# Optimization experiments

Hardware: AMD Instinct MI355X
Metric: run time of the kernel (lower is better)

## Reference

```python
import jax, jax.numpy as jnp
import numpy as np


def setup_inputs() -> dict:
    key = jax.random.key(0)
    k1, k2, k3, k4 = jax.random.split(key, 4)
    B, C, H, W = 16, 256, 64, 64
    OUT = 256
    x = jax.random.normal(k1, (B, C, H, W), dtype=jnp.float32)
    context = jax.random.normal(k2, (B, C, H, W), dtype=jnp.float32)
    # conv1: 1x1 Conv2d(in=C, out=OUT) -> weight [OUT, C], bias [OUT]
    w1 = jax.random.normal(k3, (OUT, C), dtype=jnp.float32) * (1.0 / np.sqrt(C))
    b1 = jax.random.normal(k4, (OUT,), dtype=jnp.float32) * 0.01
    return {"x": x, "context": context, "w1": w1, "b1": b1}


def reference(x, context, w1, b1):
    # AdaptiveAvgPool2d((1,1)) over context -> per-(b,c) scalar scale [B, C]
    scale = jnp.mean(context, axis=(2, 3))
    # grouped conv with groups=B*C and 1x1 kernels == per-channel elementwise scale
    depth_feat = x * scale[:, :, None, None]  # [B, C, H, W]
    # 1x1 pointwise conv: contract channel dim
    out = jnp.einsum("bchw,oc->bohw", depth_feat, w1) + b1[None, :, None, None]
    return out
```

## Files before the change

kernel.cpp:

```cpp
#include <hip/hip_runtime.h>
#include <hip/hip_bf16.h>


typedef __attribute__((ext_vector_type(8))) short short8;
typedef __attribute__((ext_vector_type(4))) float f32x4;
typedef __attribute__((ext_vector_type(4))) unsigned int u32x4;

static __device__ __forceinline__ unsigned int bfbits(float f) {
    unsigned int u = __float_as_uint(f);
    return u + 0x7FFFu + ((u >> 16) & 1u);
}

static __device__ __forceinline__ unsigned int pkbf(float lo, float hi) {
#if __has_builtin(__builtin_amdgcn_perm)
    return __builtin_amdgcn_perm(bfbits(hi), bfbits(lo), 0x07060302u);
#else
    return (bfbits(lo) >> 16) | (bfbits(hi) & 0xffff0000u);
#endif
}

__global__ __launch_bounds__(256) void scale_kernel(const float* __restrict__ ctx,
                                                    float* __restrict__ scale) {
    const int bc = blockIdx.x;
    const float4* p = (const float4*)(ctx + (size_t)bc * 4096);
    const int t = threadIdx.x;
    float s = 0.f;
#pragma unroll
    for (int k = 0; k < 4; k++) {
        float4 v = p[t + k * 256];
        s += v.x + v.y + v.z + v.w;
    }
#pragma unroll
    for (int off = 32; off > 0; off >>= 1) s += __shfl_down(s, off);
    __shared__ float ws[4];
    if ((t & 63) == 0) ws[t >> 6] = s;
    __syncthreads();
    if (t == 0) scale[bc] = (ws[0] + ws[1] + ws[2] + ws[3]) * (1.0f / 4096.0f);
}

__global__ __launch_bounds__(256) void w2f_kernel(const float* __restrict__ w1,
                                                  const float* __restrict__ scale,
                                                  unsigned short* __restrict__ w2f) {
    const int gt = blockIdx.x * 256 + threadIdx.x;
    const int lane = gt & 63;
    const int m16 = (gt >> 6) & 15;
    const int ks = (gt >> 10) & 7;
    const int b = gt >> 13;
    const int lr = lane & 15;
    const int g = lane >> 4;
    const int row = m16 * 16 + lr;
    const int c0 = ks * 32 + g * 8;

    const float* wr = w1 + row * 256 + c0;
    const float* sc = scale + b * 256 + c0;
    float4 wv0 = *(const float4*)(wr);
    float4 wv1 = *(const float4*)(wr + 4);
    float4 sv0 = *(const float4*)(sc);
    float4 sv1 = *(const float4*)(sc + 4);

    u32x4 pv;
    pv[0] = pkbf(wv0.x * sv0.x, wv0.y * sv0.y);
    pv[1] = pkbf(wv0.z * sv0.z, wv0.w * sv0.w);
    pv[2] = pkbf(wv1.x * sv1.x, wv1.y * sv1.y);
    pv[3] = pkbf(wv1.z * sv1.z, wv1.w * sv1.w);
    *(u32x4*)(w2f + (size_t)gt * 8) = pv;
}

__global__ __launch_bounds__(256, 4) void gemm_kernel(const float* __restrict__ x,
                                                      const unsigned short* __restrict__ w2f,
                                                      const float* __restrict__ b1,
                                                      float* __restrict__ out) {
    const int bid = blockIdx.x;
    const int b = bid >> 7;
    const int hw0 = (bid & 127) * 32;
    const int tid = threadIdx.x;
    const int w = tid >> 6;
    const int lane = tid & 63;
    const int g = lane >> 4;
    const int lr = lane & 15;
    const int o0 = (w & 1) * 128;
    const int cw = hw0 + (w >> 1) * 16;
    const int m16b = (w & 1) * 8;

    const unsigned short* Af = w2f + (size_t)b * 65536;
    const float* Xcol = x + (size_t)b * (256 * 4096) + cw + lr;

    f32x4 acc[8];
#pragma unroll
    for (int m = 0; m < 8; m++) acc[m] = (f32x4)(0.f);

    float bcur[8], bnxt[8];
#pragma unroll
    for (int e = 0; e < 8; e++) bcur[e] = Xcol[(size_t)(g * 8 + e) * 4096];

#pragma unroll
    for (int ks = 0; ks < 8; ks++) {
        if (ks < 7) {
#pragma unroll
            for (int e = 0; e < 8; e++)
                bnxt[e] = Xcol[(size_t)((ks + 1) * 32 + g * 8 + e) * 4096];
        }
        short8 a[8];
#pragma unroll
        for (int m = 0; m < 8; m++)
            a[m] = *(const short8*)(Af + ((size_t)(ks * 16 + m16b + m) * 64 + lane) * 8);
        u32x4 pv;
#pragma unroll
        for (int j = 0; j < 4; j++) pv[j] = pkbf(bcur[2 * j], bcur[2 * j + 1]);
        short8 bf = __builtin_bit_cast(short8, pv);
#pragma unroll
        for (int m = 0; m < 8; m++)
            acc[m] = __builtin_amdgcn_mfma_f32_16x16x32_bf16(a[m], bf, acc[m], 0, 0, 0);
#pragma unroll
        for (int e = 0; e < 8; e++) bcur[e] = bnxt[e];
    }

    float* outp = out + (size_t)b * 256 * 4096 + cw + lr;
#pragma unroll
    for (int m = 0; m < 8; m++) {
#pragma unroll
        for (int r = 0; r < 4; r++) {
            const int row = o0 + m * 16 + g * 4 + r;
            outp[(size_t)row * 4096] = acc[m][r] + b1[row];
        }
    }
}

extern "C" void kernel_launch(void* const* d_in, const int* in_sizes, int n_in,
                              void* d_out, int out_size, void* d_ws, size_t ws_size,
                              hipStream_t stream) {
    const float* x = (const float*)d_in[0];
    const float* context = (const float*)d_in[1];
    const float* w1 = (const float*)d_in[2];
    const float* b1 = (const float*)d_in[3];
    float* out = (float*)d_out;

    float* scale = (float*)d_ws;
    unsigned short* w2f = (unsigned short*)((char*)d_ws + 16384);

    scale_kernel<<<4096, 256, 0, stream>>>(context, scale);
    w2f_kernel<<<512, 256, 0, stream>>>(w1, scale, w2f);
    gemm_kernel<<<2048, 256, 0, stream>>>(x, w2f, b1, out);
}
```

Before: 51.52 us.

## Stage X tiles in LDS via async global_load_lds and switch to 32x32 MFMA

The GEMM now uses 64-column output tiles per block (half the grid). It loads X tiles into double-buffered shared memory with direct global-to-LDS loads, and uses 32x32x16 bf16 MFMAs with a 2x2 accumulator tile per wave. The weight pre-pack kernel is re-laid out to match the 32x32 fragment layout. This aims to coalesce X reads and raise MFMA efficiency, at the cost of 32KB LDS per block, block-level barriers and lower occupancy.

After: 42.49 us. -17.5%, faster.

```diff
diff --git a/kernel.cpp b/kernel.cpp
--- a/kernel.cpp
+++ b/kernel.cpp
@@ -3,7 +3,7 @@
 
 
 typedef __attribute__((ext_vector_type(8))) short short8;
-typedef __attribute__((ext_vector_type(4))) float f32x4;
+typedef __attribute__((ext_vector_type(16))) float f32x16;
 typedef __attribute__((ext_vector_type(4))) unsigned int u32x4;
 
 static __device__ __forceinline__ unsigned int bfbits(float f) {
@@ -17,6 +17,12 @@
 #else
     return (bfbits(lo) >> 16) | (bfbits(hi) & 0xffff0000u);
 #endif
+}
+
+static __device__ __forceinline__ void gload16(const void* g, void* l) {
+    __builtin_amdgcn_global_load_lds(
+        (const __attribute__((address_space(1))) unsigned int*)g,
+        (__attribute__((address_space(3))) unsigned int*)l, 16, 0, 0);
 }
 
 __global__ __launch_bounds__(256) void scale_kernel(const float* __restrict__ ctx,
@@ -42,14 +48,12 @@
                                                   const float* __restrict__ scale,
                                                   unsigned short* __restrict__ w2f) {
     const int gt = blockIdx.x * 256 + threadIdx.x;
-    const int lane = gt & 63;
-    const int m16 = (gt >> 6) & 15;
-    const int ks = (gt >> 10) & 7;
+    const int l = gt & 63;
+    const int mt = (gt >> 6) & 7;
+    const int ks = (gt >> 9) & 15;
     const int b = gt >> 13;
-    const int lr = lane & 15;
-    const int g = lane >> 4;
-    const int row = m16 * 16 + lr;
-    const int c0 = ks * 32 + g * 8;
+    const int row = mt * 32 + (l & 31);
+    const int c0 = ks * 16 + (l >> 5) * 8;
 
     const float* wr = w1 + row * 256 + c0;
     const float* sc = scale + b * 256 + c0;
@@ -66,64 +70,91 @@
     *(u32x4*)(w2f + (size_t)gt * 8) = pv;
 }
 
-__global__ __launch_bounds__(256, 4) void gemm_kernel(const float* __restrict__ x,
+__global__ __launch_bounds__(256, 3) void gemm_kernel(const float* __restrict__ x,
                                                       const unsigned short* __restrict__ w2f,
                                                       const float* __restrict__ b1,
                                                       float* __restrict__ out) {
+    __shared__ float bst[2][4096];
+
     const int bid = blockIdx.x;
-    const int b = bid >> 7;
-    const int hw0 = (bid & 127) * 32;
+    const int b = bid >> 6;
+    const int hw0 = (bid & 63) * 64;
     const int tid = threadIdx.x;
     const int w = tid >> 6;
     const int lane = tid & 63;
-    const int g = lane >> 4;
-    const int lr = lane & 15;
-    const int o0 = (w & 1) * 128;
-    const int cw = hw0 + (w >> 1) * 16;
-    const int m16b = (w & 1) * 8;
+    const int l31 = lane & 31;
+    const int lh = lane >> 5;
+    const int o0 = w * 64;
 
     const unsigned short* Af = w2f + (size_t)b * 65536;
-    const float* Xcol = x + (size_t)b * (256 * 4096) + cw + lr;
-
-    f32x4 acc[8];
-#pragma unroll
-    for (int m = 0; m < 8; m++) acc[m] = (f32x4)(0.f);
-
-    float bcur[8], bnxt[8];
-#pragma unroll
-    for (int e = 0; e < 8; e++) bcur[e] = Xcol[(size_t)(g * 8 + e) * 4096];
+    const float* Xb = x + (size_t)b * (256 * 4096) + hw0;
 
 #pragma unroll
-    for (int ks = 0; ks < 8; ks++) {
-        if (ks < 7) {
+    for (int i = 0; i < 4; i++) {
+        const int idx = i * 256 + tid;
+        gload16(Xb + (size_t)(idx >> 4) * 4096 + (idx & 15) * 4, &bst[0][idx * 4]);
+    }
+    __syncthreads();
+
+    f32x16 acc[2][2];
 #pragma unroll
-            for (int e = 0; e < 8; e++)
-                bnxt[e] = Xcol[(size_t)((ks + 1) * 32 + g * 8 + e) * 4096];
+    for (int mtl = 0; mtl < 2; mtl++)
+#pragma unroll
+        for (int ntl = 0; ntl < 2; ntl++) acc[mtl][ntl] = (f32x16)(0.f);
+
+    const int bbase = lh * 512 + l31;
+
+#pragma unroll
+    for (int kt = 0; kt < 4; kt++) {
+        if (kt < 3) {
+#pragma unroll
+            for (int i = 0; i < 4; i++) {
+                const int idx = i * 256 + tid;
+                gload16(Xb + (size_t)((kt + 1) * 64 + (idx >> 4)) * 4096 + (idx & 15) * 4,
+                        &bst[(kt + 1) & 1][idx * 4]);
+            }
         }
-        short8 a[8];
+        const float* bb = bst[kt & 1];
+
+        short8 a[4][2];
 #pragma unroll
-        for (int m = 0; m < 8; m++)
-            a[m] = *(const short8*)(Af + ((size_t)(ks * 16 + m16b + m) * 64 + lane) * 8);
-        u32x4 pv;
+        for (int sub = 0; sub < 4; sub++)
 #pragma unroll
-        for (int j = 0; j < 4; j++) pv[j] = pkbf(bcur[2 * j], bcur[2 * j + 1]);
-        short8 bf = __builtin_bit_cast(short8, pv);
+            for (int mtl = 0; mtl < 2; mtl++)
+                a[sub][mtl] = *(const short8*)(
+                    Af + (((size_t)(kt * 4 + sub) * 8 + (w * 2 + mtl)) * 64 + lane) * 8);
+
 #pragma unroll
-        for (int m = 0; m < 8; m++)
-            acc[m] = __builtin_amdgcn_mfma_f32_16x16x32_bf16(a[m], bf, acc[m], 0, 0, 0);
+        for (int sub = 0; sub < 4; sub++) {
 #pragma unroll
-        for (int e = 0; e < 8; e++) bcur[e] = bnxt[e];
+            for (int ntl = 0; ntl < 2; ntl++) {
+                float bf32[8];
+#pragma unroll
+                for (int e = 0; e < 8; e++)
+                    bf32[e] = bb[bbase + ntl * 32 + sub * 1024 + e * 64];
+                u32x4 pv;
+#pragma unroll
+                for (int j = 0; j < 4; j++) pv[j] = pkbf(bf32[2 * j], bf32[2 * j + 1]);
+                short8 bfr = __builtin_bit_cast(short8, pv);
+#pragma unroll
+                for (int mtl = 0; mtl < 2; mtl++)
+                    acc[mtl][ntl] = __builtin_amdgcn_mfma_f32_32x32x16_bf16(
+                        a[sub][mtl], bfr, acc[mtl][ntl], 0, 0, 0);
+            }
+        }
+        __syncthreads();
     }
 
-    float* outp = out + (size_t)b * 256 * 4096 + cw + lr;
+    float* outb = out + (size_t)b * 256 * 4096 + hw0;
 #pragma unroll
-    for (int m = 0; m < 8; m++) {
+    for (int mtl = 0; mtl < 2; mtl++)
 #pragma unroll
-        for (int r = 0; r < 4; r++) {
-            const int row = o0 + m * 16 + g * 4 + r;
-            outp[(size_t)row * 4096] = acc[m][r] + b1[row];
-        }
-    }
+        for (int ntl = 0; ntl < 2; ntl++)
+#pragma unroll
+            for (int r = 0; r < 16; r++) {
+                const int row = o0 + mtl * 32 + (r & 3) + 8 * (r >> 2) + 4 * lh;
+                outb[(size_t)row * 4096 + ntl * 32 + l31] = acc[mtl][ntl][r] + b1[row];
+            }
 }
 
 extern "C" void kernel_launch(void* const* d_in, const int* in_sizes, int n_in,
@@ -140,5 +171,5 @@
 
     scale_kernel<<<4096, 256, 0, stream>>>(context, scale);
     w2f_kernel<<<512, 256, 0, stream>>>(w1, scale, w2f);
-    gemm_kernel<<<2048, 256, 0, stream>>>(x, w2f, b1, out);
+    gemm_kernel<<<1024, 256, 0, stream>>>(x, w2f, b1, out);
 }
```

## Switch GEMM to 32x32x16 MFMA tiles with XCD-aware block remapping

Applied to the files above, without the earlier changes.

The pointwise-conv GEMM now uses 32x32x16 bf16 MFMA instead of 16x16x32. Each wave covers 32 spatial columns and 128 output channels, and each block covers 128 columns and one half of the output channels. The weight pre-pack kernel is changed to emit the matching 32x32 A-fragment layout. Block IDs are remapped so each XCD gets contiguous work, and the two channel halves that read the same x columns sit on the same XCD. This widens coalesced x reads and output writes to 32 lanes and aims to share x in L2. In exchange the grid is halved, which lowers occupancy, and x is still read by two blocks.

New measurement: 47.32 us. 1.09x faster.

```diff
diff --git a/kernel.cpp b/kernel.cpp
--- a/kernel.cpp
+++ b/kernel.cpp
@@ -3,7 +3,7 @@
 
 
 typedef __attribute__((ext_vector_type(8))) short short8;
-typedef __attribute__((ext_vector_type(4))) float f32x4;
+typedef __attribute__((ext_vector_type(16))) float f32x16;
 typedef __attribute__((ext_vector_type(4))) unsigned int u32x4;
 
 static __device__ __forceinline__ unsigned int bfbits(float f) {
@@ -42,14 +42,12 @@
                                                   const float* __restrict__ scale,
                                                   unsigned short* __restrict__ w2f) {
     const int gt = blockIdx.x * 256 + threadIdx.x;
-    const int lane = gt & 63;
-    const int m16 = (gt >> 6) & 15;
-    const int ks = (gt >> 10) & 7;
+    const int l = gt & 63;
+    const int mt = (gt >> 6) & 7;
+    const int ks = (gt >> 9) & 15;
     const int b = gt >> 13;
-    const int lr = lane & 15;
-    const int g = lane >> 4;
-    const int row = m16 * 16 + lr;
-    const int c0 = ks * 32 + g * 8;
+    const int row = mt * 32 + (l & 31);
+    const int c0 = ks * 16 + (l >> 5) * 8;
 
     const float* wr = w1 + row * 256 + c0;
     const float* sc = scale + b * 256 + c0;
@@ -71,57 +69,58 @@
                                                       const float* __restrict__ b1,
                                                       float* __restrict__ out) {
     const int bid = blockIdx.x;
-    const int b = bid >> 7;
-    const int hw0 = (bid & 127) * 32;
+    const int work = (bid & 7) * 128 + (bid >> 3);
+    const int b = work >> 6;
+    const int rh = (work >> 5) & 1;
+    const int cg = work & 31;
     const int tid = threadIdx.x;
     const int w = tid >> 6;
     const int lane = tid & 63;
-    const int g = lane >> 4;
-    const int lr = lane & 15;
-    const int o0 = (w & 1) * 128;
-    const int cw = hw0 + (w >> 1) * 16;
-    const int m16b = (w & 1) * 8;
+    const int l31 = lane & 31;
+    const int lh = lane >> 5;
+    const int cw = cg * 128 + w * 32;
 
     const unsigned short* Af = w2f + (size_t)b * 65536;
-    const float* Xcol = x + (size_t)b * (256 * 4096) + cw + lr;
+    const float* Xcol = x + (size_t)b * (256 * 4096) + cw + l31;
 
-    f32x4 acc[8];
+    f32x16 acc[4];
 #pragma unroll
-    for (int m = 0; m < 8; m++) acc[m] = (f32x4)(0.f);
+    for (int mt = 0; mt < 4; mt++) acc[mt] = (f32x16)(0.f);
 
     float bcur[8], bnxt[8];
 #pragma unroll
-    for (int e = 0; e < 8; e++) bcur[e] = Xcol[(size_t)(g * 8 + e) * 4096];
+    for (int e = 0; e < 8; e++) bcur[e] = Xcol[(size_t)(lh * 8 + e) * 4096];
 
 #pragma unroll
-    for (int ks = 0; ks < 8; ks++) {
-        if (ks < 7) {
+    for (int kt = 0; kt < 16; kt++) {
+        if (kt < 15) {
 #pragma unroll
             for (int e = 0; e < 8; e++)
-                bnxt[e] = Xcol[(size_t)((ks + 1) * 32 + g * 8 + e) * 4096];
+                bnxt[e] = Xcol[(size_t)((kt + 1) * 16 + lh * 8 + e) * 4096];
         }
-        short8 a[8];
+        short8 a[4];
 #pragma unroll
-        for (int m = 0; m < 8; m++)
-            a[m] = *(const short8*)(Af + ((size_t)(ks * 16 + m16b + m) * 64 + lane) * 8);
+        for (int mt = 0; mt < 4; mt++)
+            a[mt] = *(const short8*)(
+                Af + (((size_t)kt * 8 + rh * 4 + mt) * 64 + lane) * 8);
         u32x4 pv;
 #pragma unroll
         for (int j = 0; j < 4; j++) pv[j] = pkbf(bcur[2 * j], bcur[2 * j + 1]);
-        short8 bf = __builtin_bit_cast(short8, pv);
+        short8 bfr = __builtin_bit_cast(short8, pv);
 #pragma unroll
-        for (int m = 0; m < 8; m++)
-            acc[m] = __builtin_amdgcn_mfma_f32_16x16x32_bf16(a[m], bf, acc[m], 0, 0, 0);
+        for (int mt = 0; mt < 4; mt++)
+            acc[mt] = __builtin_amdgcn_mfma_f32_32x32x16_bf16(a[mt], bfr, acc[mt], 0, 0, 0);
 #pragma unroll
         for (int e = 0; e < 8; e++) bcur[e] = bnxt[e];
     }
 
-    float* outp = out + (size_t)b * 256 * 4096 + cw + lr;
+    float* outp = out + (size_t)b * 256 * 4096 + cw + l31;
 #pragma unroll
-    for (int m = 0; m < 8; m++) {
+    for (int mt = 0; mt < 4; mt++) {
 #pragma unroll
-        for (int r = 0; r < 4; r++) {
-            const int row = o0 + m * 16 + g * 4 + r;
-            outp[(size_t)row * 4096] = acc[m][r] + b1[row];
+        for (int r = 0; r < 16; r++) {
+            const int row = rh * 128 + mt * 32 + (r & 3) + 8 * (r >> 2) + 4 * lh;
+            outp[(size_t)row * 4096] = acc[mt][r] + b1[row];
         }
     }
 }
@@ -140,5 +139,5 @@
 
     scale_kernel<<<4096, 256, 0, stream>>>(context, scale);
     w2f_kernel<<<512, 256, 0, stream>>>(w1, scale, w2f);
-    gemm_kernel<<<2048, 256, 0, stream>>>(x, w2f, b1, out);
+    gemm_kernel<<<1024, 256, 0, stream>>>(x, w2f, b1, out);
 }
```
